# Kernel tuning notes

Measured on AMD Instinct MI355X. Metric: run time of the kernel, lower is better.

The kernel has to match this reference:

```python
import jax, jax.numpy as jnp
import numpy as np

D_IN = 1024
D_OUT = 1024
N_HEADS = 16
HEAD_DIM = D_IN // N_HEADS      # 64
HEAD_DIM_V = D_OUT // N_HEADS   # 64


def setup_inputs() -> dict:
    key = jax.random.key(0)
    ks = jax.random.split(key, 7)
    s = 0.02
    x = jax.random.normal(ks[0], (4, 2048, D_IN), dtype=jnp.float32)
    Wq = jax.random.normal(ks[1], (D_IN, D_IN), dtype=jnp.float32) * s
    bq = jnp.zeros((D_IN,), dtype=jnp.float32)
    Wk = jax.random.normal(ks[2], (D_IN, D_IN), dtype=jnp.float32) * s
    bk = jnp.zeros((D_IN,), dtype=jnp.float32)
    Wv = jax.random.normal(ks[3], (D_IN, D_OUT), dtype=jnp.float32) * s
    bv = jnp.zeros((D_OUT,), dtype=jnp.float32)
    return {"x": x, "Wq": Wq, "bq": bq, "Wk": Wk, "bk": bk, "Wv": Wv, "bv": bv}


def reference(x, Wq, bq, Wk, bk, Wv, bv):
    B, S, _ = x.shape
    scale = jnp.sqrt(jnp.asarray(HEAD_DIM, dtype=jnp.float32))
    # projections -> [B, S, H, Dh] -> [B, H, S, Dh]
    q = (x @ Wq + bq).reshape(B, S, N_HEADS, HEAD_DIM).transpose(0, 2, 1, 3)
    k = (x @ Wk + bk).reshape(B, S, N_HEADS, HEAD_DIM).transpose(0, 2, 1, 3)
    v = (x @ Wv + bv).reshape(B, S, N_HEADS, HEAD_DIM_V).transpose(0, 2, 1, 3)
    # [B, H, S, S] attention scores (naive full materialization, as in source)
    scores = jnp.einsum("bhsd,bhtd->bhst", q, k) / scale
    weights = jax.nn.softmax(scores, axis=-1)
    out = jnp.einsum("bhst,bhtd->bhsd", weights, v)
    # [B, H, S, Dv] -> [B, S, H*Dv]  (out_projection NOT applied in source forward)
    return out.transpose(0, 2, 1, 3).reshape(B, S, N_HEADS * HEAD_DIM_V)
```

## Files before the change

### kernel.cpp

```cpp
#include <hip/hip_runtime.h>

#define B_  4
#define S_  2048
#define D_  1024
#define H_  16
#define DH_ 64
#define M_  (B_ * S_)

typedef __attribute__((ext_vector_type(8))) short short8;
typedef __attribute__((ext_vector_type(4))) float floatx4;

__device__ __forceinline__ unsigned short f2bf(float f) {
    union { float f; unsigned int i; } v; v.f = f;
    unsigned int r = v.i + 0x7fffu + ((v.i >> 16) & 1u);
    return (unsigned short)(r >> 16);
}
__device__ __forceinline__ unsigned int pk_trunc(float a, float b) {
#if __has_builtin(__builtin_amdgcn_perm)
    return __builtin_amdgcn_perm(__float_as_uint(b), __float_as_uint(a), 0x07060302u);
#else
    return (__float_as_uint(a) >> 16) | (__float_as_uint(b) & 0xffff0000u);
#endif
}

#if __has_builtin(__builtin_amdgcn_exp2f)
#define EXP2(x) __builtin_amdgcn_exp2f(x)
#else
#define EXP2(x) __expf(0.6931471805599453f * (x))
#endif

typedef const __attribute__((address_space(1))) unsigned int* gas_ptr;
typedef __attribute__((address_space(3))) unsigned int* las_ptr;
__device__ __forceinline__ void async_cp16(const void* g, void* l) {
    __builtin_amdgcn_global_load_lds((gas_ptr)g, (las_ptr)l, 16, 0, 0);
}

#define VMC3 asm volatile("s_waitcnt vmcnt(3)" ::: "memory")
#define VMC0 asm volatile("s_waitcnt vmcnt(0)" ::: "memory")

__global__ __launch_bounds__(256) void cast_fused_kernel(
    const float* __restrict__ x, unsigned short* __restrict__ Ax,
    const float* __restrict__ W0, const float* __restrict__ W1,
    const float* __restrict__ W2,
    unsigned short* __restrict__ T0, unsigned short* __restrict__ T1,
    unsigned short* __restrict__ T2)
{
    const int bid = blockIdx.x;
    const int t = threadIdx.x;
    if (bid < 8192) {
        int i4 = bid * 256 + t;
        float4 v = reinterpret_cast<const float4*>(x)[i4];
        ushort4 o;
        o.x = f2bf(v.x); o.y = f2bf(v.y); o.z = f2bf(v.z); o.w = f2bf(v.w);
        reinterpret_cast<ushort4*>(Ax)[i4] = o;
        return;
    }
    const int idx = bid - 8192;
    const int z   = idx >> 8;
    const int rem = idx & 255;
    const float* W = z == 0 ? W0 : (z == 1 ? W1 : W2);
    unsigned short* Wt = z == 0 ? T0 : (z == 1 ? T1 : T2);

    __shared__ unsigned short T[64][72];
    const int k0 = (rem & 15) * 64, n0 = (rem >> 4) * 64;

    #pragma unroll
    for (int p = 0; p < 4; ++p) {
        int kr = p * 16 + (t >> 4);
        int nc = (t & 15) * 4;
        float4 v = *reinterpret_cast<const float4*>(W + (size_t)(k0 + kr) * D_ + n0 + nc);
        T[nc + 0][kr] = f2bf(v.x);
        T[nc + 1][kr] = f2bf(v.y);
        T[nc + 2][kr] = f2bf(v.z);
        T[nc + 3][kr] = f2bf(v.w);
    }
    __syncthreads();

    const int nl = t >> 2, kc = (t & 3) * 16;
    size_t base = (size_t)(n0 + nl) * D_ + k0 + kc;
    *reinterpret_cast<short8*>(Wt + base)     = *reinterpret_cast<const short8*>(&T[nl][kc]);
    *reinterpret_cast<short8*>(Wt + base + 8) = *reinterpret_cast<const short8*>(&T[nl][kc + 8]);
}

__global__ __launch_bounds__(512) void gemm_qkv_mfma(
    const unsigned short* __restrict__ Ax,
    const unsigned short* __restrict__ Wt,
    const float* __restrict__ bq, const float* __restrict__ bk,
    const float* __restrict__ bv,
    unsigned short* __restrict__ Q,
    unsigned short* __restrict__ Vtg)
{
    __shared__ unsigned short lds[49152];

    const int tid  = threadIdx.x;
    const int lane = tid & 63;
    const int w    = tid >> 6;
    const int wm   = w >> 2;
    const int wn   = w & 3;
    const int l15  = lane & 15, quad = lane >> 4;

    const int pl   = tid >> 3;
    const int sl   = tid & 7;
    const int xx   = sl ^ (pl & 7);
    const int sro  = pl * 2 + (xx >> 2);
    const int sc   = (xx & 3) * 8;
    const int ldst = tid * 8;
    const int fb = (l15 >> 1) * 64 + ((((l15 & 1) << 2) | quad) ^ (l15 >> 1)) * 8;

    const int id  = blockIdx.x;
    const int g   = (id & 7) * 96 + (id >> 3);
    const int nb  = g >> 6;
    const int mb  = g & 63;
    const int m0  = mb * 128;
    const int n0g = nb * 256;
    const int mat = nb >> 2;
    const int n0m = (nb & 3) * 256;
    const float* bias = mat == 0 ? bq : (mat == 1 ? bk : bv);

    #define ASTG(kcol, reg) \
        async_cp16(Ax + (size_t)(m0 + sro) * 1024 + (kcol) + sc, lds + (reg) + ldst)
    #define BSTG(kcol, reg) do { \
        async_cp16(Wt + (size_t)(n0g + sro) * 1024 + (kcol) + sc,       lds + (reg) + ldst); \
        async_cp16(Wt + (size_t)(n0g + 128 + sro) * 1024 + (kcol) + sc, lds + (reg) + 4096 + ldst); \
    } while (0)

    floatx4 acc[4][4] = {};

    ASTG(0, 0);      BSTG(0, 8192);
    ASTG(32, 4096);  BSTG(32, 16384);
    ASTG(64, 24576); BSTG(64, 32768);
    VMC3;
    __builtin_amdgcn_s_barrier();

    #define PH(bufS, ksub, STAGE_STMT, WAIT_STMT) do { \
        short8 af[4], bfr[4]; \
        _Pragma("unroll") \
        for (int i = 0; i < 4; ++i) \
            af[i] = *reinterpret_cast<const short8*>(lds + (bufS) + (ksub) * 4096 + wm * 2048 + i * 512 + fb); \
        _Pragma("unroll") \
        for (int j = 0; j < 4; ++j) \
            bfr[j] = *reinterpret_cast<const short8*>(lds + (bufS) + 8192 + (ksub) * 8192 + wn * 2048 + j * 512 + fb); \
        STAGE_STMT; \
        __builtin_amdgcn_s_barrier(); \
        asm volatile("s_waitcnt lgkmcnt(0)" ::: "memory"); \
        __builtin_amdgcn_sched_barrier(0); \
        __builtin_amdgcn_s_setprio(1); \
        _Pragma("unroll") \
        for (int i = 0; i < 4; ++i) \
            _Pragma("unroll") \
            for (int j = 0; j < 4; ++j) \
                acc[i][j] = __builtin_amdgcn_mfma_f32_16x16x32_bf16(af[i], bfr[j], acc[i][j], 0, 0, 0); \
        __builtin_amdgcn_s_setprio(0); \
        WAIT_STMT; \
        __builtin_amdgcn_s_barrier(); \
    } while (0)

    #pragma unroll 1
    for (int it = 0; it < 8; ++it) {
        const bool nl = (it < 7);
        const int  kA = (2 * it + 1) * 64;
        const int  kB = kA + 64;
        const int  kC = kA + 128;
        PH(0,     0, { ASTG(kA + 32, 28672); BSTG(kA + 32, 40960); }, );
        PH(0,     1, if (nl) { ASTG(kB, 0); BSTG(kB, 8192); }, { if (nl) VMC3; else VMC0; });
        PH(24576, 0, if (nl) { ASTG(kB + 32, 4096); BSTG(kB + 32, 16384); }, );
        PH(24576, 1, if (nl) { ASTG(kC, 24576); BSTG(kC, 32768); }, { if (nl) VMC3; });
    }

    float bb[4];
    #pragma unroll
    for (int j = 0; j < 4; ++j) bb[j] = bias[n0m + wn * 64 + j * 16 + l15];

    if (mat == 2) {
        const int bI    = m0 >> 11;
        #pragma unroll
        for (int i = 0; i < 4; ++i) {
            int srow = (m0 & 2047) + wm * 64 + i * 16 + quad * 4;
            #pragma unroll
            for (int j = 0; j < 4; ++j) {
                int col = n0m + wn * 64 + j * 16 + l15;
                ushort4 o;
                o.x = f2bf(acc[i][j][0] + bb[j]);
                o.y = f2bf(acc[i][j][1] + bb[j]);
                o.z = f2bf(acc[i][j][2] + bb[j]);
                o.w = f2bf(acc[i][j][3] + bb[j]);
                *reinterpret_cast<ushort4*>(Vtg + (size_t)(bI * 1024 + col) * S_ + srow) = o;
            }
        }
    } else {
        unsigned short* C = Q + (size_t)mat * M_ * D_;
        const float scq = (mat == 0) ? 0.18033688011112042f : 1.0f;
        #pragma unroll
        for (int i = 0; i < 4; ++i)
            #pragma unroll
            for (int r = 0; r < 4; ++r) {
                int row = m0 + wm * 64 + i * 16 + quad * 4 + r;
                #pragma unroll
                for (int j = 0; j < 4; ++j)
                    C[(size_t)row * D_ + n0m + wn * 64 + j * 16 + l15] = f2bf((acc[i][j][r] + bb[j]) * scq);
            }
    }
}

#define KT_   64
#define NT_   (S_ / KT_)
#define SWZ(row, col) ((((row) << 6)) + ((col) ^ (((row) & 7) << 3)))

__global__ __launch_bounds__(256, 4) void attn_mfma(
    const unsigned short* __restrict__ Qg,
    const unsigned short* __restrict__ Kg,
    const unsigned short* __restrict__ Vtg,
    float* __restrict__ out)
{
    __shared__ unsigned short Ks[KT_ * 64];
    __shared__ unsigned short Vt[DH_ * 64];

    const int tid  = threadIdx.x;
    const int wq   = tid >> 6;
    const int lane = tid & 63;
    const int l15  = lane & 15;
    const int quad = lane >> 4;

    const int id  = blockIdx.x;
    const int bh  = (id & 7) * 8 + ((id >> 3) & 7);
    const int qt  = id >> 6;
    const int b   = bh >> 4;
    const int colbase = (bh & 15) * DH_;
    const int rowQ0 = b * S_ + qt * 128;

    short8 qf[2][2];
    #pragma unroll
    for (int g = 0; g < 2; ++g) {
        int qrow = rowQ0 + wq * 32 + g * 16 + l15;
        qf[g][0] = *reinterpret_cast<const short8*>(Qg + (size_t)qrow * D_ + colbase + quad * 8);
        qf[g][1] = *reinterpret_cast<const short8*>(Qg + (size_t)qrow * D_ + colbase + 32 + quad * 8);
    }

    short8 vones;
    #pragma unroll
    for (int i = 0; i < 8; ++i) vones[i] = (short)0x3F80;

    floatx4 Oacc[2][4] = {};
    floatx4 Lacc[2] = {};

    const int srow = tid >> 3;
    const int sc8  = (tid & 7) * 8;
    const int vc  = sc8 >> 4;
    const int vqk = (sc8 >> 2) & 3;
    const int vk0 = ((vc & 1) << 2) + ((vc >> 1) << 5) + (vqk << 3);

    const unsigned short* Kbase = Kg + (size_t)(b * S_) * D_ + colbase;
    const unsigned short* Vbase = Vtg + (size_t)(bh * 64) * S_;

    short8 kpre[2], vpre[2];
    #pragma unroll
    for (int p = 0; p < 2; ++p) {
        kpre[p] = *reinterpret_cast<const short8*>(Kbase + (size_t)(p * 32 + srow) * D_ + sc8);
        vpre[p] = *reinterpret_cast<const short8*>(Vbase + (size_t)(p * 32 + srow) * S_ + sc8);
    }

    for (int kt = 0; kt < NT_; ++kt) {
        __syncthreads();
        #pragma unroll
        for (int p = 0; p < 2; ++p) {
            int r = p * 32 + srow;
            *reinterpret_cast<short8*>(&Ks[SWZ(r, sc8)]) = kpre[p];
            uint4 u = __builtin_bit_cast(uint4, vpre[p]);
            uint2 lo, hi;
            lo.x = u.x; lo.y = u.y; hi.x = u.z; hi.y = u.w;
            *reinterpret_cast<uint2*>(&Vt[SWZ(r, vk0)])     = lo;
            *reinterpret_cast<uint2*>(&Vt[SWZ(r, vk0 + 8)]) = hi;
        }
        __syncthreads();
        if (kt + 1 < NT_) {
            int off = (kt + 1) * KT_;
            #pragma unroll
            for (int p = 0; p < 2; ++p) {
                kpre[p] = *reinterpret_cast<const short8*>(Kbase + (size_t)(off + p * 32 + srow) * D_ + sc8);
                vpre[p] = *reinterpret_cast<const short8*>(Vbase + (size_t)(p * 32 + srow) * S_ + off + sc8);
            }
        }

        #pragma unroll
        for (int half = 0; half < 2; ++half) {
            floatx4 s_[2][2];
            __builtin_amdgcn_s_setprio(1);
            #pragma unroll
            for (int ci = 0; ci < 2; ++ci) {
                int c = half * 2 + ci;
                int kr = c * 16 + l15;
                short8 kf0 = *reinterpret_cast<const short8*>(&Ks[SWZ(kr, quad * 8)]);
                short8 kf1 = *reinterpret_cast<const short8*>(&Ks[SWZ(kr, 32 + quad * 8)]);
                #pragma unroll
                for (int g = 0; g < 2; ++g) {
                    floatx4 a = {0.f, 0.f, 0.f, 0.f};
                    a = __builtin_amdgcn_mfma_f32_16x16x32_bf16(kf0, qf[g][0], a, 0, 0, 0);
                    a = __builtin_amdgcn_mfma_f32_16x16x32_bf16(kf1, qf[g][1], a, 0, 0, 0);
                    s_[g][ci] = a;
                }
            }
            __builtin_amdgcn_s_setprio(0);
            short8 pa[2];
            #pragma unroll
            for (int g = 0; g < 2; ++g) {
                float p00 = EXP2(s_[g][0][0]), p01 = EXP2(s_[g][0][1]);
                float p02 = EXP2(s_[g][0][2]), p03 = EXP2(s_[g][0][3]);
                float p10 = EXP2(s_[g][1][0]), p11 = EXP2(s_[g][1][1]);
                float p12 = EXP2(s_[g][1][2]), p13 = EXP2(s_[g][1][3]);
                uint4 pu;
                pu.x = pk_trunc(p00, p01);
                pu.y = pk_trunc(p02, p03);
                pu.z = pk_trunc(p10, p11);
                pu.w = pk_trunc(p12, p13);
                pa[g] = __builtin_bit_cast(short8, pu);
            }
            __builtin_amdgcn_s_setprio(1);
            #pragma unroll
            for (int g = 0; g < 2; ++g)
                Lacc[g] = __builtin_amdgcn_mfma_f32_16x16x32_bf16(pa[g], vones, Lacc[g], 0, 0, 0);
            #pragma unroll
            for (int d = 0; d < 4; ++d) {
                int vr = d * 16 + l15;
                short8 vf = *reinterpret_cast<const short8*>(&Vt[SWZ(vr, half * 32 + quad * 8)]);
                #pragma unroll
                for (int g = 0; g < 2; ++g)
                    Oacc[g][d] = __builtin_amdgcn_mfma_f32_16x16x32_bf16(pa[g], vf, Oacc[g][d], 0, 0, 0);
            }
            __builtin_amdgcn_s_setprio(0);
        }
    }

    #pragma unroll
    for (int g = 0; g < 2; ++g) {
        int orow = rowQ0 + wq * 32 + g * 16 + quad * 4;
        #pragma unroll
        for (int r = 0; r < 4; ++r) {
            float inv = 1.f / Lacc[g][r];
            #pragma unroll
            for (int d = 0; d < 4; ++d)
                out[(size_t)(orow + r) * D_ + colbase + d * 16 + l15] = Oacc[g][d][r] * inv;
        }
    }
}

extern "C" void kernel_launch(void* const* d_in, const int* in_sizes, int n_in,
                              void* d_out, int out_size, void* d_ws, size_t ws_size,
                              hipStream_t stream) {
    const float* x  = (const float*)d_in[0];
    const float* Wq = (const float*)d_in[1];
    const float* bq = (const float*)d_in[2];
    const float* Wk = (const float*)d_in[3];
    const float* bk = (const float*)d_in[4];
    const float* Wv = (const float*)d_in[5];
    const float* bv = (const float*)d_in[6];
    float* out = (float*)d_out;

    unsigned short* Q   = (unsigned short*)d_ws;
    unsigned short* K   = Q + (size_t)M_ * D_;
    unsigned short* Vtg = K + (size_t)M_ * D_;
    unsigned short* Ax  = Vtg + (size_t)M_ * D_;
    unsigned short* Wtq = Ax + (size_t)M_ * D_;
    unsigned short* Wtk = Wtq + (size_t)D_ * D_;
    unsigned short* Wtv = Wtk + (size_t)D_ * D_;

    cast_fused_kernel<<<8192 + 768, 256, 0, stream>>>(x, Ax, Wq, Wk, Wv, Wtq, Wtk, Wtv);

    gemm_qkv_mfma<<<768, 512, 0, stream>>>(Ax, Wtq, bq, bk, bv, Q, Vtg);

    attn_mfma<<<1024, 256, 0, stream>>>(Q, K, Vtg, out);
}
```

Baseline: 233.7 us.

## Widen QKV GEMM tile to 128x384 with per-column matrix routing

The fused QKV projection GEMM tile grows from 128x256 to 128x384, so each block now issues 6 B-fragments per wave and the grid shrinks from 768 to 512 blocks. This gives exactly two blocks per CU on 256 CUs and improves reuse of the A tile. Because a 384-wide tile can cross the Q/K/V boundary, the epilogue now picks the target matrix and bias per 16-column group. The LDS footprint grows to 128KB per block, the wait counts are adjusted for the extra load, and accumulator register pressure rises.

```diff
diff --git a/kernel.cpp b/kernel.cpp
--- a/kernel.cpp
+++ b/kernel.cpp
@@ -35,7 +35,7 @@
     __builtin_amdgcn_global_load_lds((gas_ptr)g, (las_ptr)l, 16, 0, 0);
 }
 
-#define VMC3 asm volatile("s_waitcnt vmcnt(3)" ::: "memory")
+#define VMC4 asm volatile("s_waitcnt vmcnt(4)" ::: "memory")
 #define VMC0 asm volatile("s_waitcnt vmcnt(0)" ::: "memory")
 
 __global__ __launch_bounds__(256) void cast_fused_kernel(
@@ -82,7 +82,7 @@
     *reinterpret_cast<short8*>(Wt + base + 8) = *reinterpret_cast<const short8*>(&T[nl][kc + 8]);
 }
 
-__global__ __launch_bounds__(512) void gemm_qkv_mfma(
+__global__ __launch_bounds__(512, 2) void gemm_qkv_mfma(
     const unsigned short* __restrict__ Ax,
     const unsigned short* __restrict__ Wt,
     const float* __restrict__ bq, const float* __restrict__ bk,
@@ -90,7 +90,7 @@
     unsigned short* __restrict__ Q,
     unsigned short* __restrict__ Vtg)
 {
-    __shared__ unsigned short lds[49152];
+    __shared__ unsigned short lds[65536];
 
     const int tid  = threadIdx.x;
     const int lane = tid & 63;
@@ -104,42 +104,39 @@
     const int xx   = sl ^ (pl & 7);
     const int sro  = pl * 2 + (xx >> 2);
     const int sc   = (xx & 3) * 8;
-    const int ldst = tid * 8;
     const int fb = (l15 >> 1) * 64 + ((((l15 & 1) << 2) | quad) ^ (l15 >> 1)) * 8;
 
     const int id  = blockIdx.x;
-    const int g   = (id & 7) * 96 + (id >> 3);
+    const int g   = (id & 7) * 64 + (id >> 3);
     const int nb  = g >> 6;
     const int mb  = g & 63;
     const int m0  = mb * 128;
-    const int n0g = nb * 256;
-    const int mat = nb >> 2;
-    const int n0m = (nb & 3) * 256;
-    const float* bias = mat == 0 ? bq : (mat == 1 ? bk : bv);
+    const int n0g = nb * 384;
 
     #define ASTG(kcol, reg) \
-        async_cp16(Ax + (size_t)(m0 + sro) * 1024 + (kcol) + sc, lds + (reg) + ldst)
+        async_cp16(Ax + (size_t)(m0 + sro) * 1024 + (kcol) + sc, lds + (reg) + tid * 8)
     #define BSTG(kcol, reg) do { \
-        async_cp16(Wt + (size_t)(n0g + sro) * 1024 + (kcol) + sc,       lds + (reg) + ldst); \
-        async_cp16(Wt + (size_t)(n0g + 128 + sro) * 1024 + (kcol) + sc, lds + (reg) + 4096 + ldst); \
+        async_cp16(Wt + (size_t)(n0g + sro) * 1024 + (kcol) + sc,       lds + (reg) + tid * 8); \
+        async_cp16(Wt + (size_t)(n0g + 128 + sro) * 1024 + (kcol) + sc, lds + (reg) + 4096 + tid * 8); \
+        async_cp16(Wt + (size_t)(n0g + 256 + sro) * 1024 + (kcol) + sc, lds + (reg) + 8192 + tid * 8); \
     } while (0)
 
-    floatx4 acc[4][4] = {};
+    floatx4 acc[4][6] = {};
 
     ASTG(0, 0);      BSTG(0, 8192);
-    ASTG(32, 4096);  BSTG(32, 16384);
-    ASTG(64, 24576); BSTG(64, 32768);
-    VMC3;
+    ASTG(32, 4096);  BSTG(32, 20480);
+    ASTG(64, 32768); BSTG(64, 40960);
+    VMC4;
     __builtin_amdgcn_s_barrier();
 
     #define PH(bufS, ksub, STAGE_STMT, WAIT_STMT) do { \
-        short8 af[4], bfr[4]; \
+        short8 af[4], bfr[6]; \
         _Pragma("unroll") \
         for (int i = 0; i < 4; ++i) \
             af[i] = *reinterpret_cast<const short8*>(lds + (bufS) + (ksub) * 4096 + wm * 2048 + i * 512 + fb); \
         _Pragma("unroll") \
-        for (int j = 0; j < 4; ++j) \
-            bfr[j] = *reinterpret_cast<const short8*>(lds + (bufS) + 8192 + (ksub) * 8192 + wn * 2048 + j * 512 + fb); \
+        for (int j = 0; j < 6; ++j) \
+            bfr[j] = *reinterpret_cast<const short8*>(lds + (bufS) + 8192 + (ksub) * 12288 + (wn * 6 + j) * 512 + fb); \
         STAGE_STMT; \
         __builtin_amdgcn_s_barrier(); \
         asm volatile("s_waitcnt lgkmcnt(0)" ::: "memory"); \
@@ -148,7 +145,7 @@
         _Pragma("unroll") \
         for (int i = 0; i < 4; ++i) \
             _Pragma("unroll") \
-            for (int j = 0; j < 4; ++j) \
+            for (int j = 0; j < 6; ++j) \
                 acc[i][j] = __builtin_amdgcn_mfma_f32_16x16x32_bf16(af[i], bfr[j], acc[i][j], 0, 0, 0); \
         __builtin_amdgcn_s_setprio(0); \
         WAIT_STMT; \
@@ -161,44 +158,42 @@
         const int  kA = (2 * it + 1) * 64;
         const int  kB = kA + 64;
         const int  kC = kA + 128;
-        PH(0,     0, { ASTG(kA + 32, 28672); BSTG(kA + 32, 40960); }, );
-        PH(0,     1, if (nl) { ASTG(kB, 0); BSTG(kB, 8192); }, { if (nl) VMC3; else VMC0; });
-        PH(24576, 0, if (nl) { ASTG(kB + 32, 4096); BSTG(kB + 32, 16384); }, );
-        PH(24576, 1, if (nl) { ASTG(kC, 24576); BSTG(kC, 32768); }, { if (nl) VMC3; });
-    }
-
-    float bb[4];
-    #pragma unroll
-    for (int j = 0; j < 4; ++j) bb[j] = bias[n0m + wn * 64 + j * 16 + l15];
-
-    if (mat == 2) {
-        const int bI    = m0 >> 11;
-        #pragma unroll
-        for (int i = 0; i < 4; ++i) {
-            int srow = (m0 & 2047) + wm * 64 + i * 16 + quad * 4;
-            #pragma unroll
-            for (int j = 0; j < 4; ++j) {
-                int col = n0m + wn * 64 + j * 16 + l15;
+        PH(0,     0, { ASTG(kA + 32, 36864); BSTG(kA + 32, 53248); }, );
+        PH(0,     1, if (nl) { ASTG(kB, 0); BSTG(kB, 8192); }, { if (nl) VMC4; else VMC0; });
+        PH(32768, 0, if (nl) { ASTG(kB + 32, 4096); BSTG(kB + 32, 20480); }, );
+        PH(32768, 1, if (nl) { ASTG(kC, 32768); BSTG(kC, 40960); }, { if (nl) VMC4; });
+    }
+
+    const int bI    = m0 >> 11;
+    const int sbase = (m0 & 2047) + wm * 64;
+    #pragma unroll
+    for (int j = 0; j < 6; ++j) {
+        const int gc0 = n0g + wn * 96 + j * 16;
+        const int mt  = gc0 >> 10;
+        const int cm  = (gc0 & 1023) + l15;
+        const float bb = (mt == 0 ? bq : (mt == 1 ? bk : bv))[cm];
+        if (mt == 2) {
+            #pragma unroll
+            for (int i = 0; i < 4; ++i) {
+                int srow = sbase + i * 16 + quad * 4;
                 ushort4 o;
-                o.x = f2bf(acc[i][j][0] + bb[j]);
-                o.y = f2bf(acc[i][j][1] + bb[j]);
-                o.z = f2bf(acc[i][j][2] + bb[j]);
-                o.w = f2bf(acc[i][j][3] + bb[j]);
-                *reinterpret_cast<ushort4*>(Vtg + (size_t)(bI * 1024 + col) * S_ + srow) = o;
-            }
-        }
-    } else {
-        unsigned short* C = Q + (size_t)mat * M_ * D_;
-        const float scq = (mat == 0) ? 0.18033688011112042f : 1.0f;
-        #pragma unroll
-        for (int i = 0; i < 4; ++i)
-            #pragma unroll
-            for (int r = 0; r < 4; ++r) {
-                int row = m0 + wm * 64 + i * 16 + quad * 4 + r;
+                o.x = f2bf(acc[i][j][0] + bb);
+                o.y = f2bf(acc[i][j][1] + bb);
+                o.z = f2bf(acc[i][j][2] + bb);
+                o.w = f2bf(acc[i][j][3] + bb);
+                *reinterpret_cast<ushort4*>(Vtg + (size_t)(bI * 1024 + cm) * S_ + srow) = o;
+            }
+        } else {
+            unsigned short* C = Q + (size_t)mt * M_ * D_;
+            const float scq = (mt == 0) ? 0.18033688011112042f : 1.0f;
+            #pragma unroll
+            for (int i = 0; i < 4; ++i)
                 #pragma unroll
-                for (int j = 0; j < 4; ++j)
-                    C[(size_t)row * D_ + n0m + wn * 64 + j * 16 + l15] = f2bf((acc[i][j][r] + bb[j]) * scq);
-            }
+                for (int r = 0; r < 4; ++r) {
+                    int row = m0 + wm * 64 + i * 16 + quad * 4 + r;
+                    C[(size_t)row * D_ + cm] = f2bf((acc[i][j][r] + bb) * scq);
+                }
+        }
     }
 }
 
@@ -365,7 +360,7 @@
 
     cast_fused_kernel<<<8192 + 768, 256, 0, stream>>>(x, Ax, Wq, Wk, Wv, Wtq, Wtk, Wtv);
 
-    gemm_qkv_mfma<<<768, 512, 0, stream>>>(Ax, Wtq, bq, bk, bv, Q, Vtg);
+    gemm_qkv_mfma<<<512, 512, 0, stream>>>(Ax, Wtq, bq, bk, bv, Q, Vtg);
 
     attn_mfma<<<1024, 256, 0, stream>>>(Q, K, Vtg, out);
 }
```

New measurement: 235.9 us. Within noise of the previous version (+0.9%).
